# Kernel tuning notes

Measured on AMD Instinct MI355X. Metric: run time of the kernel, lower is better.

Reference implementation:

```python
import jax, jax.numpy as jnp
import numpy as np
from jax import lax

IMAGENET_MEAN = jnp.array([0.485, 0.456, 0.406], dtype=jnp.float32).reshape(1, 3, 1, 1)
IMAGENET_STD = jnp.array([0.229, 0.224, 0.225], dtype=jnp.float32).reshape(1, 3, 1, 1)
MAX_ITERS = 10
TEMPERATURE = 500.0


def conv3x3(x, w, b):
    # NCHW conv, stride 1, padding 1 (same as nn.Conv2d(k=3, padding=1))
    y = lax.conv_general_dilated(x, w, (1, 1), ((1, 1), (1, 1)),
                                 dimension_numbers=("NCHW", "OIHW", "NCHW"))
    return y + b[None, :, None, None]


def setup_inputs() -> dict:
    key = jax.random.key(0)
    k = jax.random.split(key, 8)
    B, H, W = 8, 512, 512
    real_img = jax.random.uniform(k[0], (B, 3, H, W), dtype=jnp.float32)
    pred_img = jax.random.uniform(k[1], (B, 3, H, W), dtype=jnp.float32)
    mask = jax.random.uniform(k[2], (B, 1, H, W), dtype=jnp.float32)
    # VGG19 first two convs (random-init stand-ins, scaled like kaiming-ish)
    w1 = jax.random.normal(k[3], (64, 3, 3, 3), dtype=jnp.float32) * 0.1
    b1 = jax.random.normal(k[4], (64,), dtype=jnp.float32) * 0.01
    w2 = jax.random.normal(k[5], (64, 64, 3, 3), dtype=jnp.float32) * 0.05
    b2 = jax.random.normal(k[6], (64,), dtype=jnp.float32) * 0.01
    erode_w = jnp.ones((1, 1, 3, 3), dtype=jnp.float32)  # weight.data.fill_(1)
    return {"real_img": real_img, "pred_img": pred_img, "mask": mask,
            "w1": w1, "b1": b1, "w2": w2, "b2": b2, "erode_w": erode_w}


def _forward(real_img, pred_img, mask, w1, b1, w2, b2, erode_w):
    x = (real_img - IMAGENET_MEAN) / IMAGENET_STD
    # features = conv1_1 -> relu -> conv1_2 -> relu (level=2, no pooling reached)
    f = jax.nn.relu(conv3x3(x, w1, b1))
    real_feats = jax.nn.relu(conv3x3(f, w2, b2))  # [B,64,H,W]

    dv = real_feats[:, :, 1:, :] - real_feats[:, :, :-1, :]
    vertical_sim = jnp.exp(-jnp.sum(dv * dv, axis=1, keepdims=True) / TEMPERATURE)  # [B,1,H-1,W]
    dh = real_feats[:, :, :, 1:] - real_feats[:, :, :, :-1]
    horizontal_sim = jnp.exp(-jnp.sum(dh * dh, axis=1, keepdims=True) / TEMPERATURE)  # [B,1,H,W-1]

    B, _, Hf, Wf = real_feats.shape
    # bilinear resize, half-pixel centers == F.interpolate(align_corners=False)
    mask_scaled = jax.image.resize(mask, (B, 1, Hf, Wf), method="bilinear")
    # erode: all-ones 3x3 conv (zero pad), threshold > 1
    eroded = lax.conv_general_dilated(mask_scaled, erode_w, (1, 1), ((1, 1), (1, 1)),
                                      dimension_numbers=("NCHW", "OIHW", "NCHW"))
    mask_scaled = (eroded > 1.0).astype(jnp.float32)

    cur0 = 1.0 - mask_scaled

    def body(i, cur):
        top = cur[:, :, :-1, :] * vertical_sim
        new_top = jnp.concatenate([top[:, :, :1, :], top], axis=2)  # replicate pad top
        bot = cur[:, :, 1:, :] * vertical_sim
        new_bot = jnp.concatenate([bot, bot[:, :, -1:, :]], axis=2)  # replicate pad bottom
        lef = cur[:, :, :, :-1] * horizontal_sim
        new_lef = jnp.concatenate([lef[:, :, :, :1], lef], axis=3)  # replicate pad left
        rig = cur[:, :, :, 1:] * horizontal_sim
        new_rig = jnp.concatenate([rig, rig[:, :, :, -1:]], axis=3)  # replicate pad right
        new_know = jnp.maximum(jnp.maximum(new_top, new_bot), jnp.maximum(new_lef, new_rig))
        return jnp.maximum(cur, new_know)

    cur_knowness = lax.fori_loop(0, MAX_ITERS, body, cur0)

    Hm, Wm = mask.shape[-2:]
    cur_knowness = jax.image.resize(cur_knowness, (B, 1, Hm, Wm), method="bilinear")
    return jnp.minimum(mask, 1.0 - cur_knowness)


def reference(real_img, pred_img, mask, w1, b1, w2, b2, erode_w):
    return _forward(real_img, pred_img, mask, w1, b1, w2, b2, erode_w)
```

## Files before the change

kernel.cpp:

```cpp
#include <hip/hip_runtime.h>
#include <hip/hip_bf16.h>

#define HH 512
#define WW 512
#define NB 8
#define IMG (HH*WW)
#define TS 15
#define NTL 35

typedef __bf16 bf16x8 __attribute__((ext_vector_type(8)));
typedef float  f32x4  __attribute__((ext_vector_type(4)));

__device__ __forceinline__ float bflo(unsigned u){ return __uint_as_float(u << 16); }
__device__ __forceinline__ float bfhi(unsigned u){ return __uint_as_float(u & 0xffff0000u); }
__device__ __forceinline__ unsigned f2bf_bits(float f){
    union { float f; unsigned u; } v; v.f = f;
    return (v.u + 0x7fffu + ((v.u >> 16) & 1u)) >> 16;
}
__device__ __forceinline__ unsigned packbf(float lo, float hi){
    return f2bf_bits(lo) | (f2bf_bits(hi) << 16);
}
__device__ __forceinline__ unsigned cvtpk(float lo, float hi){
    unsigned r;
    asm("v_cvt_pk_bf16_f32 %0, %1, %2" : "=v"(r) : "v"(lo), "v"(hi));
    return r;
}

__global__ void prep_kernel(const float* __restrict__ w2, const float* __restrict__ w1,
                            uint4* __restrict__ wb, uint4* __restrict__ wa)
{
    int i = blockIdx.x * 256 + threadIdx.x;
    if (i < 9*2*4*64){
        int tap = i >> 9;
        int rem = i & 511;
        int ks  = rem >> 8;
        int nf  = (rem >> 6) & 3;
        int l   = rem & 63;
        int oc  = nf*16 + (l & 15);
        int icb = ks*32 + (l >> 4)*8;
        float v[8];
        #pragma unroll
        for (int j = 0; j < 8; ++j)
            v[j] = w2[(oc*64 + icb + j)*9 + tap];
        uint4 q;
        q.x = packbf(v[0], v[1]); q.y = packbf(v[2], v[3]);
        q.z = packbf(v[4], v[5]); q.w = packbf(v[6], v[7]);
        wb[i] = q;
    } else if (i < 9*2*4*64 + 4*64){
        int idx = i - 9*2*4*64;
        int mf = idx >> 6, l = idx & 63;
        int oc = mf*16 + (l & 15);
        int kb = (l >> 4)*8;
        float v[8];
        #pragma unroll
        for (int j = 0; j < 8; ++j)
            v[j] = (kb + j < 27) ? w1[oc*27 + kb + j] : 0.f;
        uint4 q;
        q.x = packbf(v[0], v[1]); q.y = packbf(v[2], v[3]);
        q.z = packbf(v[4], v[5]); q.w = packbf(v[6], v[7]);
        wa[idx] = q;
    }
}

__global__ __launch_bounds__(256, 2)
void conv_sims_kernel(const float* __restrict__ img,
                      const float* __restrict__ b1,
                      const uint4* __restrict__ wa,
                      const uint4* __restrict__ wb, const float* __restrict__ b2,
                      float* __restrict__ vs, float* __restrict__ hs)
{
    __shared__ float xs[3][20][20];
    __shared__ uint4 fs4[8*324];
    __shared__ uint4 uni[2048];

    const int tid = threadIdx.x;
    const int bid = blockIdx.x;
    const int b   = bid / (NTL*NTL);
    const int t2  = bid % (NTL*NTL);
    const int th  = t2 / NTL, tw = t2 % NTL;
    const int h0  = th * TS, w0 = tw * TS;

    for (int i = tid; i < 3*20*20; i += 256){
        int ic = i / 400, r = (i / 20) % 20, c = i % 20;
        int gy = h0 - 2 + r, gx = w0 - 2 + c;
        float mean = (ic == 0) ? 0.485f : (ic == 1) ? 0.456f : 0.406f;
        float istd = (ic == 0) ? (1.f/0.229f) : (ic == 1) ? (1.f/0.224f) : (1.f/0.225f);
        float v = 0.f;
        if (gy >= 0 && gy < HH && gx >= 0 && gx < WW)
            v = (img[(b*3 + ic)*IMG + gy*WW + gx] - mean) * istd;
        xs[ic][r][c] = v;
    }
    __syncthreads();

    {
        for (int p = tid; p < 336; p += 256){
            uint4 c0 = {0,0,0,0}, c1 = c0, c2 = c0, c3 = c0;
            if (p < 324){
                int fy = p / 18, fx = p % 18;
                float xv[27];
                #pragma unroll
                for (int ic = 0; ic < 3; ++ic)
                    #pragma unroll
                    for (int ky = 0; ky < 3; ++ky)
                        #pragma unroll
                        for (int kx = 0; kx < 3; ++kx)
                            xv[ic*9 + ky*3 + kx] = xs[ic][fy + ky][fx + kx];
                c0.x = cvtpk(xv[0], xv[1]);  c0.y = cvtpk(xv[2], xv[3]);
                c0.z = cvtpk(xv[4], xv[5]);  c0.w = cvtpk(xv[6], xv[7]);
                c1.x = cvtpk(xv[8], xv[9]);  c1.y = cvtpk(xv[10], xv[11]);
                c1.z = cvtpk(xv[12], xv[13]);c1.w = cvtpk(xv[14], xv[15]);
                c2.x = cvtpk(xv[16], xv[17]);c2.y = cvtpk(xv[18], xv[19]);
                c2.z = cvtpk(xv[20], xv[21]);c2.w = cvtpk(xv[22], xv[23]);
                c3.x = cvtpk(xv[24], xv[25]);c3.y = cvtpk(xv[26], 0.f);
            }
            uni[0*336 + p] = c0;
            uni[1*336 + p] = c1;
            uni[2*336 + p] = c2;
            uni[3*336 + p] = c3;
        }
    }
    __syncthreads();

    {
        const int l  = tid & 63, wv = tid >> 6;
        const int lr = l & 15,  kg = l >> 4;
        const bf16x8* wav = (const bf16x8*)wa;
        const bf16x8* xib = (const bf16x8*)uni;

        bf16x8 af[4];
        #pragma unroll
        for (int mf = 0; mf < 4; ++mf) af[mf] = wav[(mf << 6) + l];
        f32x4 binit[4];
        #pragma unroll
        for (int mf = 0; mf < 4; ++mf)
            binit[mf] = *(const f32x4*)(b1 + mf*16 + kg*4);

        for (int nb = wv; nb < 21; nb += 4){
            int px = nb*16 + lr;
            bf16x8 bf = xib[kg*336 + px];
            int fy = px / 18, fx = px % 18;
            int gy = h0 - 1 + fy, gx = w0 - 1 + fx;
            bool inimg = (px < 324) && gy >= 0 && gy < HH && gx >= 0 && gx < WW;
            #pragma unroll
            for (int mf = 0; mf < 4; ++mf){
                f32x4 acc = __builtin_amdgcn_mfma_f32_16x16x32_bf16(af[mf], bf, binit[mf], 0, 0, 0);
                unsigned lo = 0, hi = 0;
                if (inimg){
                    lo = cvtpk(fmaxf(acc[0], 0.f), fmaxf(acc[1], 0.f));
                    hi = cvtpk(fmaxf(acc[2], 0.f), fmaxf(acc[3], 0.f));
                }
                if (px < 324){
                    char* p8 = (char*)fs4 + (((mf*2 + (kg >> 1)) * 324 + px) << 4) + ((kg & 1) << 3);
                    uint2 w2v; w2v.x = lo; w2v.y = hi;
                    *(uint2*)p8 = w2v;
                }
            }
        }
    }
    __syncthreads();

    {
        const int wv = tid >> 6;
        const int l  = tid & 63;
        const int lr = l & 15;
        const int kg = l >> 4;

        f32x4 acc[4][4];
        #pragma unroll
        for (int mf = 0; mf < 4; ++mf){
            f32x4 bv = *(const f32x4*)(b2 + mf*16 + kg*4);
            #pragma unroll
            for (int nf = 0; nf < 4; ++nf) acc[mf][nf] = bv;
        }

        const bf16x8* fsb = (const bf16x8*)fs4;
        const bf16x8* wbv = (const bf16x8*)wb;

        #pragma unroll
        for (int tap = 0; tap < 9; ++tap){
            const int dy = tap / 3, dx = tap % 3;
            #pragma unroll
            for (int ks = 0; ks < 2; ++ks){
                bf16x8 wfr[4];
                #pragma unroll
                for (int mf = 0; mf < 4; ++mf)
                    wfr[mf] = wbv[((tap*8 + ks*4 + mf) << 6) + l];
                #pragma unroll
                for (int nf = 0; nf < 4; ++nf){
                    int fpx = (wv*4 + nf + dy)*18 + lr + dx;
                    bf16x8 bfr = fsb[(ks*4 + kg)*324 + fpx];
                    #pragma unroll
                    for (int mf = 0; mf < 4; ++mf)
                        acc[mf][nf] = __builtin_amdgcn_mfma_f32_16x16x32_bf16(
                            wfr[mf], bfr, acc[mf][nf], 0, 0, 0);
                }
            }
        }

        char* ftb = (char*)uni;
        #pragma unroll
        for (int nf = 0; nf < 4; ++nf){
            int px = wv*64 + nf*16 + lr;
            #pragma unroll
            for (int mf = 0; mf < 4; ++mf){
                uint2 wv2;
                wv2.x = cvtpk(fmaxf(acc[mf][nf][0], 0.f), fmaxf(acc[mf][nf][1], 0.f));
                wv2.y = cvtpk(fmaxf(acc[mf][nf][2], 0.f), fmaxf(acc[mf][nf][3], 0.f));
                *(uint2*)(ftb + (((mf*2 + (kg >> 1)) * 256 + px) << 4) + ((kg & 1) << 3)) = wv2;
            }
        }
    }
    __syncthreads();

    const uint4* ft4 = uni;
    for (int s = tid; s < 450; s += 256){
        bool isv = (s < 225);
        int r  = isv ? s : (s - 225);
        int sy = r / 15, sx = r % 15;
        int gh = h0 + sy, gw = w0 + sx;
        if (gh >= HH || gw >= WW) continue;
        int pa = sy*16 + sx;
        int pb = isv ? (pa + 16) : (pa + 1);
        float ssd = 0.f;
        #pragma unroll
        for (int j = 0; j < 8; ++j){
            uint4 qa = ft4[j*256 + pa], qb = ft4[j*256 + pb];
            unsigned da[4] = {qa.x, qa.y, qa.z, qa.w};
            unsigned db[4] = {qb.x, qb.y, qb.z, qb.w};
            #pragma unroll
            for (int k = 0; k < 4; ++k){
                float d0 = bflo(da[k]) - bflo(db[k]);
                float d1 = bfhi(da[k]) - bfhi(db[k]);
                ssd = fmaf(d0, d0, ssd);
                ssd = fmaf(d1, d1, ssd);
            }
        }
        float sim = __expf(ssd * (-1.f/500.f));
        int o = b*IMG + gh*WW + gw;
        if (isv) vs[o] = (gh < HH-1) ? sim : 0.f;
        else     hs[o] = (gw < WW-1) ? sim : 0.f;
    }
}

template<bool FIRST, bool FINAL>
__global__ __launch_bounds__(256, 2)
void prop5_kernel(const float* __restrict__ cin, float* __restrict__ cout,
                  const float* __restrict__ vs, const float* __restrict__ hs,
                  const float* __restrict__ mask, float* __restrict__ dout)
{
    __shared__ float cu[76*78];
    __shared__ float vl[74*76];
    __shared__ float hl[74*76];

    const int tid = threadIdx.x;
    const int bid = blockIdx.x;
    const int b  = bid >> 6;
    const int ty = (bid >> 3) & 7, tx = bid & 7;
    const int gy0 = ty*64 - 5, gx0 = tx*64 - 5;
    const float* vb = vs + b*IMG;
    const float* hb = hs + b*IMG;

    for (int i = tid; i < 74*74; i += 256){
        int ly = i / 74, lx = i % 74;
        int gy = min(max(gy0 + ly, 0), 511);
        int gx = min(max(gx0 + lx, 0), 511);
        int g = gy*WW + gx, o = ly*76 + lx;
        vl[o] = vb[g];
        hl[o] = hb[g];
    }

    if (FIRST){
        const float* mb = mask + b*IMG;
        for (int i = tid; i < 76*76; i += 256){
            int ly = i / 76, lx = i % 76;
            int gy = gy0 - 1 + ly, gx = gx0 - 1 + lx;
            float v = 0.f;
            if (gy >= 0 && gy < HH && gx >= 0 && gx < WW) v = mb[gy*WW + gx];
            cu[ly*78 + lx] = v;
        }
        __syncthreads();
        float val[22];
        #pragma unroll
        for (int i = 0; i < 22; ++i){
            int px = tid + i*256;
            if (px < 74*74){
                int ly = px / 74, lx = px % 74;
                int o = ly*78 + lx;
                float s = cu[o]     + cu[o+1]   + cu[o+2]
                        + cu[o+78]  + cu[o+79]  + cu[o+80]
                        + cu[o+156] + cu[o+157] + cu[o+158];
                val[i] = (s > 1.0f) ? 0.f : 1.f;
            }
        }
        __syncthreads();
        #pragma unroll
        for (int i = 0; i < 22; ++i){
            int px = tid + i*256;
            if (px < 74*74){
                int ly = px / 74, lx = px % 74;
                int gy = gy0 + ly, gx = gx0 + lx;
                if (gy >= 0 && gy < HH && gx >= 0 && gx < WW)
                    cu[(ly+1)*78 + (lx+1)] = val[i];
            }
        }
        __syncthreads();
        for (int i = tid; i < 74*74; i += 256){
            int ly = i / 74, lx = i % 74;
            int gy = gy0 + ly, gx = gx0 + lx;
            if (gy < 0 || gy >= HH || gx < 0 || gx >= WW){
                int cly = min(max(gy, 0), 511) - gy0;
                int clx = min(max(gx, 0), 511) - gx0;
                cu[(ly+1)*78 + (lx+1)] = cu[(cly+1)*78 + (clx+1)];
            }
        }
        __syncthreads();
    } else {
        const float* cb = cin + b*IMG;
        for (int i = tid; i < 74*74; i += 256){
            int ly = i / 74, lx = i % 74;
            int gy = min(max(gy0 + ly, 0), 511);
            int gx = min(max(gx0 + lx, 0), 511);
            cu[(ly+1)*78 + (lx+1)] = cb[gy*WW + gx];
        }
        __syncthreads();
    }

    #pragma unroll
    for (int k = 1; k <= 5; ++k){
        const int S = 74 - 2*k;
        const int trips = (S*S + 255) / 256;
        float val[21];
        #pragma unroll
        for (int i = 0; i < trips; ++i){
            int px = tid + i*256;
            if (px < S*S){
                int y = px / S + k, x = px % S + k;
                int oc_ = (y + 1)*78 + (x + 1);
                int os  = y*76 + x;
                float c  = cu[oc_];
                float tp = cu[oc_ - 78] * vl[os - 76];
                float bt = cu[oc_ + 78] * vl[os];
                float lf = cu[oc_ - 1]  * hl[os - 1];
                float rg = cu[oc_ + 1]  * hl[os];
                val[i] = fmaxf(fmaxf(c, fmaxf(tp, bt)), fmaxf(lf, rg));
            }
        }
        __syncthreads();
        #pragma unroll
        for (int i = 0; i < trips; ++i){
            int px = tid + i*256;
            if (px < S*S){
                int y = px / S + k, x = px % S + k;
                cu[(y + 1)*78 + (x + 1)] = val[i];
            }
        }
        __syncthreads();
    }

    const int gyc = ty*64, gxc = tx*64;
    for (int i = tid; i < 64*64; i += 256){
        int y = i >> 6, x = i & 63;
        float v = cu[(y + 6)*78 + (x + 6)];
        int g = b*IMG + (gyc + y)*WW + (gxc + x);
        if (FINAL) dout[g] = fminf(mask[g], 1.f - v);
        else       cout[g] = v;
    }
}

extern "C" void kernel_launch(void* const* d_in, const int* in_sizes, int n_in,
                              void* d_out, int out_size, void* d_ws, size_t ws_size,
                              hipStream_t stream)
{
    const float* img  = (const float*)d_in[0];
    const float* mask = (const float*)d_in[2];
    const float* w1   = (const float*)d_in[3];
    const float* b1   = (const float*)d_in[4];
    const float* w2   = (const float*)d_in[5];
    const float* b2   = (const float*)d_in[6];
    float* out = (float*)d_out;

    float* vs   = (float*)d_ws;
    float* hsm  = vs   + NB*IMG;
    float* curB = hsm  + NB*IMG;
    uint4* wbuf = (uint4*)(curB + NB*IMG);
    uint4* wabuf = wbuf + 4608;

    prep_kernel<<<37, 256, 0, stream>>>(w2, w1, wbuf, wabuf);
    conv_sims_kernel<<<NB*NTL*NTL, 256, 0, stream>>>(img, b1, wabuf, wbuf, b2, vs, hsm);

    prop5_kernel<true,  false><<<512, 256, 0, stream>>>(curB, curB, vs, hsm, mask, out);
    prop5_kernel<false, true ><<<512, 256, 0, stream>>>(curB, curB, vs, hsm, mask, out);
}
```

Before: 394.4 us.

## Fuse two 5-step propagation kernels into one 10-step kernel with wider halo

Result: slower. 794.6 us (+101.5%).

```diff
diff --git a/kernel.cpp b/kernel.cpp
--- a/kernel.cpp
+++ b/kernel.cpp
@@ -242,128 +242,106 @@
     }
 }
 
-template<bool FIRST, bool FINAL>
-__global__ __launch_bounds__(256, 2)
-void prop5_kernel(const float* __restrict__ cin, float* __restrict__ cout,
-                  const float* __restrict__ vs, const float* __restrict__ hs,
-                  const float* __restrict__ mask, float* __restrict__ dout)
+__global__ __launch_bounds__(256, 4)
+void prop10_kernel(const float* __restrict__ vsg, const float* __restrict__ hsg,
+                   const float* __restrict__ mask, float* __restrict__ dout)
 {
-    __shared__ float cu[76*78];
-    __shared__ float vl[74*76];
-    __shared__ float hl[74*76];
+    __shared__ float cu[86*88];
 
     const int tid = threadIdx.x;
     const int bid = blockIdx.x;
     const int b  = bid >> 6;
     const int ty = (bid >> 3) & 7, tx = bid & 7;
-    const int gy0 = ty*64 - 5, gx0 = tx*64 - 5;
-    const float* vb = vs + b*IMG;
-    const float* hb = hs + b*IMG;
-
-    for (int i = tid; i < 74*74; i += 256){
-        int ly = i / 74, lx = i % 74;
-        int gy = min(max(gy0 + ly, 0), 511);
-        int gx = min(max(gx0 + lx, 0), 511);
-        int g = gy*WW + gx, o = ly*76 + lx;
-        vl[o] = vb[g];
-        hl[o] = hb[g];
-    }
-
-    if (FIRST){
-        const float* mb = mask + b*IMG;
-        for (int i = tid; i < 76*76; i += 256){
-            int ly = i / 76, lx = i % 76;
-            int gy = gy0 - 1 + ly, gx = gx0 - 1 + lx;
-            float v = 0.f;
-            if (gy >= 0 && gy < HH && gx >= 0 && gx < WW) v = mb[gy*WW + gx];
-            cu[ly*78 + lx] = v;
+    const int gyc = ty*64, gxc = tx*64;
+    const int gy0m = gyc - 11, gx0m = gxc - 11;
+    const float* mb = mask + b*IMG;
+    const float* vb = vsg + b*IMG;
+    const float* hb = hsg + b*IMG;
+
+    for (int i = tid; i < 86*86; i += 256){
+        int ly = i / 86, lx = i % 86;
+        int gy = gy0m + ly, gx = gx0m + lx;
+        float v = 0.f;
+        if (gy >= 0 && gy < HH && gx >= 0 && gx < WW) v = mb[gy*WW + gx];
+        cu[ly*88 + lx] = v;
+    }
+    __syncthreads();
+
+    float val[28];
+    #pragma unroll
+    for (int i = 0; i < 28; ++i){
+        int px = tid + i*256;
+        if (px < 84*84){
+            int j = px / 84, x = px % 84;
+            int o = j*88 + x;
+            float s = cu[o]     + cu[o+1]   + cu[o+2]
+                    + cu[o+88]  + cu[o+89]  + cu[o+90]
+                    + cu[o+176] + cu[o+177] + cu[o+178];
+            val[i] = (s > 1.f) ? 0.f : 1.f;
+        }
+    }
+    __syncthreads();
+    #pragma unroll
+    for (int i = 0; i < 28; ++i){
+        int px = tid + i*256;
+        if (px < 84*84){
+            int j = px / 84, x = px % 84;
+            int gy = gyc - 10 + j, gx = gxc - 10 + x;
+            if (gy >= 0 && gy < HH && gx >= 0 && gx < WW)
+                cu[(j+1)*88 + (x+1)] = val[i];
+        }
+    }
+    __syncthreads();
+    for (int i = tid; i < 84*84; i += 256){
+        int j = i / 84, x = i % 84;
+        int gy = gyc - 10 + j, gx = gxc - 10 + x;
+        if (gy < 0 || gy >= HH || gx < 0 || gx >= WW){
+            int cj = min(max(gy, 0), 511) - (gyc - 10);
+            int cx = min(max(gx, 0), 511) - (gxc - 10);
+            cu[(j+1)*88 + (x+1)] = cu[(cj+1)*88 + (cx+1)];
+        }
+    }
+    __syncthreads();
+
+    for (int k = 1; k <= 10; ++k){
+        #pragma unroll
+        for (int i = 0; i < 28; ++i){
+            int px = tid + i*256;
+            if (px < 84*84){
+                int j = px / 84, x = px % 84;
+                bool act = (j >= k) && (j < 84-k) && (x >= k) && (x < 84-k);
+                if (act){
+                    int o = (j+1)*88 + (x+1);
+                    int gy = gyc - 10 + j, gx = gxc - 10 + x;
+                    int cgy  = min(max(gy, 0), 511),  cgym = min(max(gy-1, 0), 511);
+                    int cgx  = min(max(gx, 0), 511),  cgxm = min(max(gx-1, 0), 511);
+                    float c  = cu[o];
+                    float tp = cu[o-88] * vb[cgym*WW + cgx];
+                    float bt = cu[o+88] * vb[cgy *WW + cgx];
+                    float lf = cu[o-1]  * hb[cgy *WW + cgxm];
+                    float rg = cu[o+1]  * hb[cgy *WW + cgx];
+                    val[i] = fmaxf(fmaxf(c, fmaxf(tp, bt)), fmaxf(lf, rg));
+                }
+            }
         }
         __syncthreads();
-        float val[22];
-        #pragma unroll
-        for (int i = 0; i < 22; ++i){
+        #pragma unroll
+        for (int i = 0; i < 28; ++i){
             int px = tid + i*256;
-            if (px < 74*74){
-                int ly = px / 74, lx = px % 74;
-                int o = ly*78 + lx;
-                float s = cu[o]     + cu[o+1]   + cu[o+2]
-                        + cu[o+78]  + cu[o+79]  + cu[o+80]
-                        + cu[o+156] + cu[o+157] + cu[o+158];
-                val[i] = (s > 1.0f) ? 0.f : 1.f;
+            if (px < 84*84){
+                int j = px / 84, x = px % 84;
+                bool act = (j >= k) && (j < 84-k) && (x >= k) && (x < 84-k);
+                if (act) cu[(j+1)*88 + (x+1)] = val[i];
             }
         }
         __syncthreads();
-        #pragma unroll
-        for (int i = 0; i < 22; ++i){
-            int px = tid + i*256;
-            if (px < 74*74){
-                int ly = px / 74, lx = px % 74;
-                int gy = gy0 + ly, gx = gx0 + lx;
-                if (gy >= 0 && gy < HH && gx >= 0 && gx < WW)
-                    cu[(ly+1)*78 + (lx+1)] = val[i];
-            }
-        }
-        __syncthreads();
-        for (int i = tid; i < 74*74; i += 256){
-            int ly = i / 74, lx = i % 74;
-            int gy = gy0 + ly, gx = gx0 + lx;
-            if (gy < 0 || gy >= HH || gx < 0 || gx >= WW){
-                int cly = min(max(gy, 0), 511) - gy0;
-                int clx = min(max(gx, 0), 511) - gx0;
-                cu[(ly+1)*78 + (lx+1)] = cu[(cly+1)*78 + (clx+1)];
-            }
-        }
-        __syncthreads();
-    } else {
-        const float* cb = cin + b*IMG;
-        for (int i = tid; i < 74*74; i += 256){
-            int ly = i / 74, lx = i % 74;
-            int gy = min(max(gy0 + ly, 0), 511);
-            int gx = min(max(gx0 + lx, 0), 511);
-            cu[(ly+1)*78 + (lx+1)] = cb[gy*WW + gx];
-        }
-        __syncthreads();
-    }
-
-    #pragma unroll
-    for (int k = 1; k <= 5; ++k){
-        const int S = 74 - 2*k;
-        const int trips = (S*S + 255) / 256;
-        float val[21];
-        #pragma unroll
-        for (int i = 0; i < trips; ++i){
-            int px = tid + i*256;
-            if (px < S*S){
-                int y = px / S + k, x = px % S + k;
-                int oc_ = (y + 1)*78 + (x + 1);
-                int os  = y*76 + x;
-                float c  = cu[oc_];
-                float tp = cu[oc_ - 78] * vl[os - 76];
-                float bt = cu[oc_ + 78] * vl[os];
-                float lf = cu[oc_ - 1]  * hl[os - 1];
-                float rg = cu[oc_ + 1]  * hl[os];
-                val[i] = fmaxf(fmaxf(c, fmaxf(tp, bt)), fmaxf(lf, rg));
-            }
-        }
-        __syncthreads();
-        #pragma unroll
-        for (int i = 0; i < trips; ++i){
-            int px = tid + i*256;
-            if (px < S*S){
-                int y = px / S + k, x = px % S + k;
-                cu[(y + 1)*78 + (x + 1)] = val[i];
-            }
-        }
-        __syncthreads();
-    }
-
-    const int gyc = ty*64, gxc = tx*64;
+    }
+
     for (int i = tid; i < 64*64; i += 256){
         int y = i >> 6, x = i & 63;
-        float v = cu[(y + 6)*78 + (x + 6)];
+        float v = cu[(y + 11)*88 + (x + 11)];
         int g = b*IMG + (gyc + y)*WW + (gxc + x);
-        if (FINAL) dout[g] = fminf(mask[g], 1.f - v);
-        else       cout[g] = v;
+        dout[g] = fminf(mb[(gyc + y)*WW + (gxc + x)], 1.f - v);
     }
 }
 
@@ -379,15 +357,12 @@
     const float* b2   = (const float*)d_in[6];
     float* out = (float*)d_out;
 
-    float* vs   = (float*)d_ws;
-    float* hsm  = vs   + NB*IMG;
-    float* curB = hsm  + NB*IMG;
-    uint4* wbuf = (uint4*)(curB + NB*IMG);
+    float* vs    = (float*)d_ws;
+    float* hsm   = vs + NB*IMG;
+    uint4* wbuf  = (uint4*)(hsm + NB*IMG);
     uint4* wabuf = wbuf + 4608;
 
-    prep_kernel<<<37, 256, 0, stream>>>(w2, w1, wbuf, wabuf);
+    prep_kernel<<<19, 256, 0, stream>>>(w2, w1, wbuf, wabuf);
     conv_sims_kernel<<<NB*NTL*NTL, 256, 0, stream>>>(img, b1, wabuf, wbuf, b2, vs, hsm);
-
-    prop5_kernel<true,  false><<<512, 256, 0, stream>>>(curB, curB, vs, hsm, mask, out);
-    prop5_kernel<false, true ><<<512, 256, 0, stream>>>(curB, curB, vs, hsm, mask, out);
-}
+    prop10_kernel<<<512, 256, 0, stream>>>(vs, hsm, mask, out);
+}
```
